# Kernel optimization log

Measured on AMD Instinct MI355X. Metric: run time of the kernel, lower is better.

## Reference

```python
import jax, jax.numpy as jnp
import numpy as np

B, T, C, HS = 8, 4096, 1024, 128
BLOCK = 4096  # block_size; T == BLOCK here


def _pyr_mask(bs):
    # Faithful numpy translation of the torch 'pyr' buffer construction.
    h = bs // 2
    top = np.repeat(np.flip(np.tril(np.ones((h, h), np.float32)), axis=1), 2, axis=0)  # (bs, h)
    reps = np.array([2] * (h - 1) + [1])
    bot = np.concatenate(
        [np.zeros((1, h), np.float32),
         np.repeat(np.tril(np.ones((h, h), np.float32)), reps, axis=0)], axis=0)  # (bs, h)
    return np.concatenate([top, bot], axis=1)  # (bs, bs)


def setup_inputs() -> dict:
    key = jax.random.key(0)
    kx, kq, kk, kv = jax.random.split(key, 4)
    s = C ** -0.5
    x = jax.random.normal(kx, (B, T, C), jnp.float32)
    Wq = jax.random.normal(kq, (C, HS), jnp.float32) * s
    Wk = jax.random.normal(kk, (C, HS), jnp.float32) * s
    Wv = jax.random.normal(kv, (C, HS), jnp.float32) * s
    return {"x": x, "Wq": Wq, "Wk": Wk, "Wv": Wv}


def reference(x, Wq, Wk, Wv):
    Tlen = x.shape[1]
    start = (BLOCK - Tlen) // 2
    end = BLOCK + (-(BLOCK - Tlen)) // 2  # python floor-div, matches torch slicing
    mask = jnp.asarray(_pyr_mask(BLOCK)[:Tlen, start:end])  # (T, T) 0/1

    q = x @ Wq  # (B, T, HS)
    k = x @ Wk
    v = x @ Wv
    wei = jnp.einsum('btd,bsd->bts', q, k) * (HS ** -0.5)  # (B, T, T)
    wei = jnp.where(mask == 0, -jnp.inf, wei)  # bidirectional_mode == 'bi'
    wei = jax.nn.softmax(wei, axis=-1)
    # dropout p=0.0 -> identity
    return wei @ v  # (B, T, HS)
```

## Files before the change

kernel.cpp:

```cpp
#include <hip/hip_runtime.h>

typedef unsigned short u16;
typedef __attribute__((ext_vector_type(8))) short bf16x8;
typedef __attribute__((ext_vector_type(8))) unsigned short u16x8;
typedef __attribute__((ext_vector_type(4))) float f32x4;
typedef __attribute__((ext_vector_type(4))) unsigned short u16x4;

#define Bn 8
#define Tn 4096
#define Cn 1024
#define HSn 128

__device__ __forceinline__ float bf2f(u16 b) {
    unsigned u = ((unsigned)b) << 16;
    return __builtin_bit_cast(float, u);
}
__device__ __forceinline__ u16 f2bf(float f) {
    unsigned u = __builtin_bit_cast(unsigned, f);
    unsigned r = (u + 0x7fffu + ((u >> 16) & 1u)) >> 16;
    return (u16)r;
}

extern "C" __global__ __launch_bounds__(256) void head_wtrans(
    const float* __restrict__ Wq, const float* __restrict__ Wk,
    const float* __restrict__ Wv, u16* __restrict__ wt) {
    const float* W = (blockIdx.y == 0) ? Wq : (blockIdx.y == 1) ? Wk : Wv;
    const float scale =
        (blockIdx.y == 0) ? (0.08838834764831845f * 1.4426950408889634f) : 1.0f;
    u16* o = wt + (size_t)blockIdx.y * Cn * HSn;
    int tid = blockIdx.x * 256 + threadIdx.x;
    int n = tid >> 10, kk = tid & 1023;
    o[tid] = f2bf(W[kk * HSn + n] * scale);
}

extern "C" __global__ __launch_bounds__(256, 1) void head_proj(
    const float* __restrict__ x, const u16* __restrict__ wt, u16* __restrict__ qo,
    u16* __restrict__ ko, u16* __restrict__ vto) {
    __shared__ __align__(16) u16 aL[128 * 40];
    __shared__ __align__(16) u16 bL[3 * 128 * 40];
    const int tid = threadIdx.x;
    const int w = tid >> 6, l = tid & 63, quad = l >> 4, ln = l & 15;
    const int bm0 = blockIdx.x * 128;

    const f32x4 zero4 = {0.f, 0.f, 0.f, 0.f};
    f32x4 acc[3][4][4];
#pragma unroll
    for (int s = 0; s < 3; s++)
#pragma unroll
        for (int i = 0; i < 4; i++)
#pragma unroll
            for (int j = 0; j < 4; j++) acc[s][i][j] = zero4;

    const int m0w = (w & 1) * 64, n0w = (w >> 1) * 64;

    f32x4 xp[4];
    u16x8 wp[3][2];
    const int xrow[4] = {tid >> 3, (256 + tid) >> 3, (512 + tid) >> 3, (768 + tid) >> 3};
    const int xch = tid & 7;
    const int wrow[2] = {tid >> 2, (256 + tid) >> 2};
    const int wch = tid & 3;

#pragma unroll
    for (int p = 0; p < 4; p++)
        xp[p] = *(const f32x4*)(x + ((size_t)(bm0 + xrow[p])) * Cn + xch * 4);
#pragma unroll
    for (int s = 0; s < 3; s++)
#pragma unroll
        for (int p = 0; p < 2; p++)
            wp[s][p] = *(const u16x8*)(wt + (size_t)s * Cn * HSn + (size_t)wrow[p] * Cn +
                                       wch * 8);

    for (int kt = 0; kt < Cn / 32; kt++) {
        __syncthreads();
#pragma unroll
        for (int p = 0; p < 4; p++) {
            u16x4 vb;
#pragma unroll
            for (int j = 0; j < 4; j++) vb[j] = f2bf(xp[p][j]);
            *(u16x4*)(aL + xrow[p] * 40 + xch * 4) = vb;
        }
#pragma unroll
        for (int s = 0; s < 3; s++)
#pragma unroll
            for (int p = 0; p < 2; p++)
                *(u16x8*)(bL + s * 5120 + wrow[p] * 40 + wch * 8) = wp[s][p];
        if (kt + 1 < Cn / 32) {
            const int kn = (kt + 1) * 32;
#pragma unroll
            for (int p = 0; p < 4; p++)
                xp[p] = *(const f32x4*)(x + ((size_t)(bm0 + xrow[p])) * Cn + kn + xch * 4);
#pragma unroll
            for (int s = 0; s < 3; s++)
#pragma unroll
                for (int p = 0; p < 2; p++)
                    wp[s][p] = *(const u16x8*)(wt + (size_t)s * Cn * HSn +
                                               (size_t)wrow[p] * Cn + kn + wch * 8);
        }
        __syncthreads();
        bf16x8 af[4];
#pragma unroll
        for (int mi = 0; mi < 4; mi++)
            af[mi] = *(const bf16x8*)(aL + (m0w + mi * 16 + ln) * 40 + quad * 8);
#pragma unroll
        for (int s = 0; s < 3; s++) {
            bf16x8 bf[4];
#pragma unroll
            for (int ni = 0; ni < 4; ni++)
                bf[ni] =
                    *(const bf16x8*)(bL + s * 5120 + (n0w + ni * 16 + ln) * 40 + quad * 8);
#pragma unroll
            for (int mi = 0; mi < 4; mi++)
#pragma unroll
                for (int ni = 0; ni < 4; ni++)
                    acc[s][mi][ni] = __builtin_amdgcn_mfma_f32_16x16x32_bf16(
                        af[mi], bf[ni], acc[s][mi][ni], 0, 0, 0);
        }
    }
#pragma unroll
    for (int mi = 0; mi < 4; mi++)
#pragma unroll
        for (int ni = 0; ni < 4; ni++)
#pragma unroll
            for (int r = 0; r < 4; r++) {
                int grow = bm0 + m0w + mi * 16 + quad * 4 + r;
                int col = n0w + ni * 16 + ln;
                qo[(size_t)grow * HSn + col] = f2bf(acc[0][mi][ni][r]);
                ko[(size_t)grow * HSn + col] = f2bf(acc[1][mi][ni][r]);
                int bb = grow >> 12, t = grow & 4095;
                vto[((size_t)bb * HSn + col) * Tn + t] = f2bf(acc[2][mi][ni][r]);
            }
}

extern "C" __global__ __launch_bounds__(256) void head_flash(
    const u16* __restrict__ q, const u16* __restrict__ k, const u16* __restrict__ vt,
    float* __restrict__ out) {
    __shared__ __align__(16) u16 kL[64 * 136];
    __shared__ __align__(16) u16 vL[128 * 72];
    __shared__ __align__(16) u16 pL[4 * 16 * 72];
    const int tid = threadIdx.x;
    const int w = tid >> 6, l = tid & 63, quad = l >> 4, ln = l & 15;
    const int bx = blockIdx.x;
    const int half = bx >> 8, idx = bx & 255;
    const int p5 = idx & 31, b = idx >> 5;
    const int qb = half ? p5 : 63 - p5;
    const int q0 = qb * 64;
    const int qrow = q0 + w * 16;

    const int rkBase = tid >> 4, ckK = tid & 15;
    const int rvBase = tid >> 3, ckV = tid & 7;

    bf16x8 qf[4];
#pragma unroll
    for (int ks = 0; ks < 4; ks++)
        qf[ks] = *(const bf16x8*)(q + ((size_t)b * Tn + qrow + ln) * HSn + ks * 32 +
                                  quad * 8);

    const f32x4 zero4 = {0.f, 0.f, 0.f, 0.f};
    float m2 = -1e30f, l2 = 0.f;
    const int qme = qrow + ln;
    const int clo = 2047 - (qme >> 1), chi = 2047 + ((qme + 1) >> 1);
    f32x4 o[8];
#pragma unroll
    for (int dt = 0; dt < 8; dt++) o[dt] = zero4;

    const int qmax = q0 + 63;
    const int tlo = (2047 - (qmax >> 1)) >> 6;
    const int thi = (2047 + ((qmax + 1) >> 1)) >> 6;

    u16x8 pk[4], pv[4];
    {
        const int t0 = tlo * 64;
#pragma unroll
        for (int p = 0; p < 4; p++)
            pk[p] = *(const u16x8*)(k + ((size_t)b * Tn + t0 + p * 16 + rkBase) * HSn +
                                    ckK * 8);
#pragma unroll
        for (int p = 0; p < 4; p++)
            pv[p] = *(const u16x8*)(vt + ((size_t)b * HSn + p * 32 + rvBase) * Tn + t0 +
                                    ckV * 8);
    }

    for (int kt = tlo; kt <= thi; kt++) {
        const int t0 = kt * 64;
        __syncthreads();
#pragma unroll
        for (int p = 0; p < 4; p++)
            *(u16x8*)(kL + (p * 16 + rkBase) * 136 + ckK * 8) = pk[p];
#pragma unroll
        for (int p = 0; p < 4; p++)
            *(u16x8*)(vL + (p * 32 + rvBase) * 72 + ckV * 8) = pv[p];
        if (kt < thi) {
            const int t1 = t0 + 64;
#pragma unroll
            for (int p = 0; p < 4; p++)
                pk[p] = *(const u16x8*)(k + ((size_t)b * Tn + t1 + p * 16 + rkBase) * HSn +
                                        ckK * 8);
#pragma unroll
            for (int p = 0; p < 4; p++)
                pv[p] = *(const u16x8*)(vt + ((size_t)b * HSn + p * 32 + rvBase) * Tn +
                                        t1 + ckV * 8);
        }
        __syncthreads();

        f32x4 s[4];
#pragma unroll
        for (int nt = 0; nt < 4; nt++) s[nt] = zero4;
#pragma unroll
        for (int nt = 0; nt < 4; nt++) {
            int R = nt * 16 + ln;
#pragma unroll
            for (int ks = 0; ks < 4; ks++) {
                bf16x8 kf = *(const bf16x8*)(kL + R * 136 + (ks * 4 + quad) * 8);
                s[nt] = __builtin_amdgcn_mfma_f32_16x16x32_bf16(kf, qf[ks], s[nt], 0, 0, 0);
            }
        }
#pragma unroll
        for (int nt = 0; nt < 4; nt++)
#pragma unroll
            for (int r = 0; r < 4; r++) {
                int t = t0 + nt * 16 + quad * 4 + r;
                bool valid = (t >= clo) && (t <= chi);
                s[nt][r] = valid ? s[nt][r] : -1e30f;
            }
        float mc = s[0][0];
#pragma unroll
        for (int nt = 0; nt < 4; nt++)
#pragma unroll
            for (int r = 0; r < 4; r++) mc = fmaxf(mc, s[nt][r]);
        mc = fmaxf(mc, __shfl_xor(mc, 16, 64));
        mc = fmaxf(mc, __shfl_xor(mc, 32, 64));
        float mn = fmaxf(m2, mc);
        float alpha = exp2f(m2 - mn);
        m2 = mn;
        float ls = 0.f;
#pragma unroll
        for (int nt = 0; nt < 4; nt++) {
            u16x4 pb4;
#pragma unroll
            for (int r = 0; r < 4; r++) {
                float pvx = exp2f(s[nt][r] - mn);
                u16 pb = f2bf(pvx);
                ls += bf2f(pb);
                pb4[r] = pb;
            }
            *(u16x4*)(pL + w * 1152 + ln * 72 + nt * 16 + quad * 4) = pb4;
        }
        ls += __shfl_xor(ls, 16, 64);
        ls += __shfl_xor(ls, 32, 64);
        l2 = l2 * alpha + ls;
        float aR[4];
#pragma unroll
        for (int r = 0; r < 4; r++) aR[r] = __shfl(alpha, quad * 4 + r, 64);
#pragma unroll
        for (int dt = 0; dt < 8; dt++) {
            f32x4 oo = o[dt];
#pragma unroll
            for (int r = 0; r < 4; r++) oo[r] *= aR[r];
            o[dt] = oo;
        }
#pragma unroll
        for (int jt = 0; jt < 2; jt++) {
            bf16x8 pf = *(const bf16x8*)(pL + w * 1152 + ln * 72 + jt * 32 + quad * 8);
#pragma unroll
            for (int dt = 0; dt < 8; dt++) {
                int R = dt * 16 + ln;
                bf16x8 vf = *(const bf16x8*)(vL + R * 72 + (jt * 4 + quad) * 8);
                o[dt] = __builtin_amdgcn_mfma_f32_16x16x32_bf16(pf, vf, o[dt], 0, 0, 0);
            }
        }
    }
    float inv = 1.0f / l2;
    float rl[4];
#pragma unroll
    for (int r = 0; r < 4; r++) rl[r] = __shfl(inv, quad * 4 + r, 64);
#pragma unroll
    for (int dt = 0; dt < 8; dt++)
#pragma unroll
        for (int r = 0; r < 4; r++) {
            int row = qrow + quad * 4 + r;
            out[((size_t)b * Tn + row) * HSn + dt * 16 + ln] = o[dt][r] * rl[r];
        }
}

extern "C" void kernel_launch(void* const* d_in, const int* in_sizes, int n_in,
                              void* d_out, int out_size, void* d_ws, size_t ws_size,
                              hipStream_t stream) {
    const float* x = (const float*)d_in[0];
    const float* Wq = (const float*)d_in[1];
    const float* Wk = (const float*)d_in[2];
    const float* Wv = (const float*)d_in[3];
    float* outp = (float*)d_out;
    char* ws = (char*)d_ws;
    u16* wt = (u16*)(ws);
    u16* qb = (u16*)(ws + (1u << 20));
    u16* kb = (u16*)(ws + (9u << 20));
    u16* vtb = (u16*)(ws + (17u << 20));

    head_wtrans<<<dim3(512, 3), 256, 0, stream>>>(Wq, Wk, Wv, wt);
    head_proj<<<dim3(256), 256, 0, stream>>>(x, wt, qb, kb, vtb);
    head_flash<<<dim3(512), 256, 0, stream>>>(qb, kb, vtb, outp);
}
```

Baseline: 347.6 us.

## Split flash attention KV range in two chunks with separate combine kernel

```diff
diff --git a/kernel.cpp b/kernel.cpp
--- a/kernel.cpp
+++ b/kernel.cpp
@@ -129,6 +129,192 @@
                 int bb = grow >> 12, t = grow & 4095;
                 vto[((size_t)bb * HSn + col) * Tn + t] = f2bf(acc[2][mi][ni][r]);
             }
+}
+
+
+extern "C" __global__ __launch_bounds__(256) void head_flash_chunk(
+    const u16* __restrict__ q, const u16* __restrict__ k, const u16* __restrict__ vt,
+    u16* __restrict__ Opart, float* __restrict__ ml) {
+    __shared__ __align__(16) u16 kL[64 * 136];
+    __shared__ __align__(16) u16 vL[128 * 72];
+    __shared__ __align__(16) u16 pL[4 * 16 * 72];
+    const int tid = threadIdx.x;
+    const int w = tid >> 6, l = tid & 63, quad = l >> 4, ln = l & 15;
+    const int cid = blockIdx.x;
+    const int qb = 63 - (cid >> 4);
+    const int b = (cid & 15) >> 1;
+    const int half = cid & 1;
+    const int q0 = qb * 64;
+    const int qrow = q0 + w * 16;
+
+    const int rkBase = tid >> 4, ckK = tid & 15;
+    const int rvBase = tid >> 3, ckV = tid & 7;
+
+    bf16x8 qf[4];
+#pragma unroll
+    for (int ks = 0; ks < 4; ks++)
+        qf[ks] = *(const bf16x8*)(q + ((size_t)b * Tn + qrow + ln) * HSn + ks * 32 +
+                                  quad * 8);
+
+    const f32x4 zero4 = {0.f, 0.f, 0.f, 0.f};
+    float m2 = -1e30f, l2 = 0.f;
+    const int qme = qrow + ln;
+    const int clo = 2047 - (qme >> 1), chi = 2047 + ((qme + 1) >> 1);
+    f32x4 o[8];
+#pragma unroll
+    for (int dt = 0; dt < 8; dt++) o[dt] = zero4;
+
+    const int qmax = q0 + 63;
+    const int tlo = (2047 - (qmax >> 1)) >> 6;
+    const int thi = (2047 + ((qmax + 1) >> 1)) >> 6;
+    const int W = thi - tlo + 1;
+    const int c0 = (W + 1) >> 1;
+    const int kstart = half ? tlo + c0 : tlo;
+    const int kend = half ? thi : tlo + c0 - 1;
+
+    u16x8 pk[4], pv[4];
+    {
+        const int t0 = kstart * 64;
+#pragma unroll
+        for (int p = 0; p < 4; p++)
+            pk[p] = *(const u16x8*)(k + ((size_t)b * Tn + t0 + p * 16 + rkBase) * HSn +
+                                    ckK * 8);
+#pragma unroll
+        for (int p = 0; p < 4; p++)
+            pv[p] = *(const u16x8*)(vt + ((size_t)b * HSn + p * 32 + rvBase) * Tn + t0 +
+                                    ckV * 8);
+    }
+
+    for (int kt = kstart; kt <= kend; kt++) {
+        const int t0 = kt * 64;
+        __syncthreads();
+#pragma unroll
+        for (int p = 0; p < 4; p++)
+            *(u16x8*)(kL + (p * 16 + rkBase) * 136 + ckK * 8) = pk[p];
+#pragma unroll
+        for (int p = 0; p < 4; p++)
+            *(u16x8*)(vL + (p * 32 + rvBase) * 72 + ckV * 8) = pv[p];
+        if (kt < kend) {
+            const int t1 = t0 + 64;
+#pragma unroll
+            for (int p = 0; p < 4; p++)
+                pk[p] = *(const u16x8*)(k + ((size_t)b * Tn + t1 + p * 16 + rkBase) * HSn +
+                                        ckK * 8);
+#pragma unroll
+            for (int p = 0; p < 4; p++)
+                pv[p] = *(const u16x8*)(vt + ((size_t)b * HSn + p * 32 + rvBase) * Tn +
+                                        t1 + ckV * 8);
+        }
+        __syncthreads();
+
+        f32x4 s[4];
+#pragma unroll
+        for (int nt = 0; nt < 4; nt++) s[nt] = zero4;
+#pragma unroll
+        for (int nt = 0; nt < 4; nt++) {
+            int R = nt * 16 + ln;
+#pragma unroll
+            for (int ks = 0; ks < 4; ks++) {
+                bf16x8 kf = *(const bf16x8*)(kL + R * 136 + (ks * 4 + quad) * 8);
+                s[nt] = __builtin_amdgcn_mfma_f32_16x16x32_bf16(kf, qf[ks], s[nt], 0, 0, 0);
+            }
+        }
+#pragma unroll
+        for (int nt = 0; nt < 4; nt++)
+#pragma unroll
+            for (int r = 0; r < 4; r++) {
+                int t = t0 + nt * 16 + quad * 4 + r;
+                bool valid = (t >= clo) && (t <= chi);
+                s[nt][r] = valid ? s[nt][r] : -1e30f;
+            }
+        float mc = s[0][0];
+#pragma unroll
+        for (int nt = 0; nt < 4; nt++)
+#pragma unroll
+            for (int r = 0; r < 4; r++) mc = fmaxf(mc, s[nt][r]);
+        mc = fmaxf(mc, __shfl_xor(mc, 16, 64));
+        mc = fmaxf(mc, __shfl_xor(mc, 32, 64));
+        float mn = fmaxf(m2, mc);
+        float alpha = exp2f(m2 - mn);
+        m2 = mn;
+        float ls = 0.f;
+#pragma unroll
+        for (int nt = 0; nt < 4; nt++) {
+            u16x4 pb4;
+#pragma unroll
+            for (int r = 0; r < 4; r++) {
+                float pvx = exp2f(s[nt][r] - mn);
+                u16 pb = f2bf(pvx);
+                ls += bf2f(pb);
+                pb4[r] = pb;
+            }
+            *(u16x4*)(pL + w * 1152 + ln * 72 + nt * 16 + quad * 4) = pb4;
+        }
+        ls += __shfl_xor(ls, 16, 64);
+        ls += __shfl_xor(ls, 32, 64);
+        l2 = l2 * alpha + ls;
+        float aR[4];
+#pragma unroll
+        for (int r = 0; r < 4; r++) aR[r] = __shfl(alpha, quad * 4 + r, 64);
+#pragma unroll
+        for (int dt = 0; dt < 8; dt++) {
+            f32x4 oo = o[dt];
+#pragma unroll
+            for (int r = 0; r < 4; r++) oo[r] *= aR[r];
+            o[dt] = oo;
+        }
+#pragma unroll
+        for (int jt = 0; jt < 2; jt++) {
+            bf16x8 pf = *(const bf16x8*)(pL + w * 1152 + ln * 72 + jt * 32 + quad * 8);
+#pragma unroll
+            for (int dt = 0; dt < 8; dt++) {
+                int R = dt * 16 + ln;
+                bf16x8 vf = *(const bf16x8*)(vL + R * 72 + (jt * 4 + quad) * 8);
+                o[dt] = __builtin_amdgcn_mfma_f32_16x16x32_bf16(pf, vf, o[dt], 0, 0, 0);
+            }
+        }
+    }
+#pragma unroll
+    for (int dt = 0; dt < 8; dt++)
+#pragma unroll
+        for (int r = 0; r < 4; r++)
+            Opart[((size_t)cid * 64 + w * 16 + quad * 4 + r) * HSn + dt * 16 + ln] =
+                f2bf(o[dt][r]);
+    if (l < 16) {
+        ml[((size_t)cid * 64 + w * 16 + ln) * 2 + 0] = m2;
+        ml[((size_t)cid * 64 + w * 16 + ln) * 2 + 1] = l2;
+    }
+}
+
+extern "C" __global__ __launch_bounds__(256) void head_combine(
+    const u16* __restrict__ Opart, const float* __restrict__ ml,
+    float* __restrict__ out) {
+    const int bid = blockIdx.x;
+    const int qb = bid >> 3, b = bid & 7;
+    const int tid = threadIdx.x;
+    const int row = tid >> 2, dseg = (tid & 3) * 32;
+    const int cid0 = (63 - qb) * 16 + b * 2;
+    const size_t r0 = (size_t)cid0 * 64 + row, r1 = r0 + 64;
+    float m0 = ml[r0 * 2], l0 = ml[r0 * 2 + 1];
+    float m1 = ml[r1 * 2], l1 = ml[r1 * 2 + 1];
+    float ms = fmaxf(m0, m1);
+    float w0 = exp2f(m0 - ms), w1 = exp2f(m1 - ms);
+    float inv = 1.0f / (w0 * l0 + w1 * l1);
+    float* op = out + ((size_t)b * Tn + qb * 64 + row) * HSn + dseg;
+    const u16* p0 = Opart + r0 * HSn + dseg;
+    const u16* p1 = Opart + r1 * HSn + dseg;
+#pragma unroll
+    for (int j = 0; j < 4; j++) {
+        u16x8 a = *(const u16x8*)(p0 + j * 8);
+        u16x8 c = *(const u16x8*)(p1 + j * 8);
+        f32x4 o1, o2;
+#pragma unroll
+        for (int e = 0; e < 4; e++) o1[e] = (w0 * bf2f(a[e]) + w1 * bf2f(c[e])) * inv;
+#pragma unroll
+        for (int e = 0; e < 4; e++) o2[e] = (w0 * bf2f(a[4 + e]) + w1 * bf2f(c[4 + e])) * inv;
+        *(f32x4*)(op + j * 8) = o1;
+        *(f32x4*)(op + j * 8 + 4) = o2;
+    }
 }
 
 extern "C" __global__ __launch_bounds__(256) void head_flash(
@@ -145,7 +331,6 @@
     const int qb = half ? p5 : 63 - p5;
     const int q0 = qb * 64;
     const int qrow = q0 + w * 16;
-
     const int rkBase = tid >> 4, ckK = tid & 15;
     const int rvBase = tid >> 3, ckV = tid & 7;
 
@@ -154,7 +339,6 @@
     for (int ks = 0; ks < 4; ks++)
         qf[ks] = *(const bf16x8*)(q + ((size_t)b * Tn + qrow + ln) * HSn + ks * 32 +
                                   quad * 8);
-
     const f32x4 zero4 = {0.f, 0.f, 0.f, 0.f};
     float m2 = -1e30f, l2 = 0.f;
     const int qme = qrow + ln;
@@ -162,7 +346,6 @@
     f32x4 o[8];
 #pragma unroll
     for (int dt = 0; dt < 8; dt++) o[dt] = zero4;
-
     const int qmax = q0 + 63;
     const int tlo = (2047 - (qmax >> 1)) >> 6;
     const int thi = (2047 + ((qmax + 1) >> 1)) >> 6;
@@ -179,7 +362,6 @@
             pv[p] = *(const u16x8*)(vt + ((size_t)b * HSn + p * 32 + rvBase) * Tn + t0 +
                                     ckV * 8);
     }
-
     for (int kt = tlo; kt <= thi; kt++) {
         const int t0 = kt * 64;
         __syncthreads();
@@ -201,7 +383,6 @@
                                         t1 + ckV * 8);
         }
         __syncthreads();
-
         f32x4 s[4];
 #pragma unroll
         for (int nt = 0; nt < 4; nt++) s[nt] = zero4;
@@ -295,8 +476,15 @@
     u16* qb = (u16*)(ws + (1u << 20));
     u16* kb = (u16*)(ws + (9u << 20));
     u16* vtb = (u16*)(ws + (17u << 20));
+    u16* Opart = (u16*)(ws + (25u << 20));
+    float* ml = (float*)(ws + (42u << 20));
 
     head_wtrans<<<dim3(512, 3), 256, 0, stream>>>(Wq, Wk, Wv, wt);
     head_proj<<<dim3(256), 256, 0, stream>>>(x, wt, qb, kb, vtb);
-    head_flash<<<dim3(512), 256, 0, stream>>>(qb, kb, vtb, outp);
-}
+    if (ws_size >= (44ull << 20)) {
+        head_flash_chunk<<<dim3(1024), 256, 0, stream>>>(qb, kb, vtb, Opart, ml);
+        head_combine<<<dim3(512), 256, 0, stream>>>(Opart, ml, outp);
+    } else {
+        head_flash<<<dim3(512), 256, 0, stream>>>(qb, kb, vtb, outp);
+    }
+}
```

After: 327.5 us. 5.8% less time.
